# Performance work log

Hardware: AMD Instinct MI355X
Metric: run time of the kernel (lower is better)

Reference implementation:

```python
import jax, jax.numpy as jnp
import numpy as np

NUM_JOINTS = 75
COORDS = 3
HIDDEN = 256
MID = HIDDEN // 2
LN_EPS = 1e-5


def build_adjacency_matrix(num_joints=NUM_JOINTS):
    edges = []
    hand_bones = [(0, 1), (1, 2), (2, 3), (3, 4), (0, 5), (5, 6), (6, 7), (7, 8), (0, 9), (9, 10), (10, 11), (11, 12), (0, 13), (13, 14), (14, 15), (15, 16), (0, 17), (17, 18), (18, 19), (19, 20), (5, 9), (9, 13), (13, 17)]
    for i, j in hand_bones:
        edges.extend([(i, j), (j, i)])
    for i, j in hand_bones:
        edges.extend([(i + 21, j + 21), (j + 21, i + 21)])
    pose_bones = [(0, 1), (1, 2), (2, 3), (3, 7), (0, 4), (4, 5), (5, 6), (6, 8), (9, 10), (11, 12), (11, 13), (13, 15), (12, 14), (14, 16), (11, 23), (12, 24), (23, 24), (23, 25), (25, 27), (27, 29), (29, 31), (24, 26), (26, 28), (28, 30), (30, 32), (15, 17), (15, 19), (15, 21), (16, 18), (16, 20), (16, 22)]
    off = 42
    for i, j in pose_bones:
        if i < 33 and j < 33:
            edges.extend([(i + off, j + off), (j + off, i + off)])
    edges.extend([(57, 0), (0, 57), (58, 21), (21, 58)])
    A = np.zeros((num_joints, num_joints), dtype=np.float32)
    np.fill_diagonal(A, 1.0)
    for i, j in edges:
        if i < num_joints and j < num_joints:
            A[i, j] = 1.0
    deg = A.sum(axis=1)
    d = np.where(deg > 0, deg ** -0.5, 0.0).astype(np.float32)
    return (d[:, None] * A) * d[None, :]


def setup_inputs() -> dict:
    key = jax.random.key(0)
    ks = jax.random.split(key, 8)
    B = 16384
    x = jax.random.normal(ks[0], (B, NUM_JOINTS, COORDS), dtype=jnp.float32)
    A = jnp.asarray(build_adjacency_matrix())
    # Kaiming-uniform style init scales (values only need to be plausible)
    W1 = jax.random.normal(ks[1], (MID, COORDS), dtype=jnp.float32) * (1.0 / np.sqrt(COORDS))
    g1 = jnp.ones((MID,), jnp.float32)
    b1 = jnp.zeros((MID,), jnp.float32)
    W2 = jax.random.normal(ks[2], (HIDDEN, MID), dtype=jnp.float32) * (1.0 / np.sqrt(MID))
    g2 = jnp.ones((HIDDEN,), jnp.float32)
    b2 = jnp.zeros((HIDDEN,), jnp.float32)
    Wp = jax.random.normal(ks[3], (HIDDEN, COORDS), dtype=jnp.float32) * (1.0 / np.sqrt(COORDS))
    bp = jnp.zeros((HIDDEN,), jnp.float32)
    return {"x": x, "A": A, "W1": W1, "g1": g1, "b1": b1, "W2": W2, "g2": g2, "b2": b2, "Wp": Wp, "bp": bp}


def _layer_norm(h, gamma, beta):
    mu = h.mean(axis=-1, keepdims=True)
    var = ((h - mu) ** 2).mean(axis=-1, keepdims=True)
    return (h - mu) * jax.lax.rsqrt(var + LN_EPS) * gamma + beta


def _gcn(x, A, W, gamma, beta):
    # Z = A @ X @ W^T, then LayerNorm, then ReLU
    h = jnp.einsum('ij,bjc->bic', A, x)
    h = jnp.einsum('bic,oc->bio', h, W)
    return jax.nn.relu(_layer_norm(h, gamma, beta))


def reference(x, A, W1, g1, b1, W2, g2, b2, Wp, bp):
    # skip: per-frame mean of a linear projection of raw coords
    skip = (jnp.einsum('bjc,oc->bjo', x, Wp) + bp).mean(axis=1)  # (B, H)
    h = _gcn(x, A, W1, g1, b1)    # (B, 75, 128)
    h = _gcn(h, A, W2, g2, b2)    # (B, 75, 256)
    return h.mean(axis=1) + skip  # (B, 256)
```

## Files before the change

### kernel.cpp

```cpp
#include <hip/hip_runtime.h>

typedef __bf16 bf16;
typedef __bf16 bf16x4 __attribute__((ext_vector_type(4)));
typedef __bf16 bf16x8 __attribute__((ext_vector_type(8)));
typedef float  f32x2  __attribute__((ext_vector_type(2)));
typedef float  f32x4  __attribute__((ext_vector_type(4)));
typedef unsigned int u32;
typedef u32 u32x2 __attribute__((ext_vector_type(2)));
typedef u32 u32x4 __attribute__((ext_vector_type(4)));
typedef unsigned short u16;

#define NJ 75
#define SA 104
#define SH 104
#define SG 136
#define SX 104
#define SR 88
#define LN_EPS 1e-5f
#define MFMA16(a,b,c) __builtin_amdgcn_mfma_f32_16x16x32_bf16((a),(b),(c),0,0,0)

static __device__ __forceinline__ f32x4 f4z(){ f32x4 v={0.f,0.f,0.f,0.f}; return v; }
static __device__ __forceinline__ u32 pk2(float a, float b){
  u32 ua = (u32)__builtin_bit_cast(u16,(bf16)a);
  u32 ub = (u32)__builtin_bit_cast(u16,(bf16)b);
  return ua | (ub<<16);
}
static __device__ __forceinline__ float lo16f(u32 u){ return __uint_as_float(u<<16); }
static __device__ __forceinline__ float hi16f(u32 u){ return __uint_as_float(u & 0xffff0000u); }

template<int C>
static __device__ __forceinline__ float dppterm(float v){
  return __int_as_float(__builtin_amdgcn_update_dpp(0, __float_as_int(v), C, 0xF, 0xF, true));
}
static __device__ __forceinline__ float red16(float v){
  v += dppterm<0xB1>(v);
  v += dppterm<0x4E>(v);
  v += dppterm<0x141>(v);
  v += dppterm<0x140>(v);
  return v;
}

__global__ __launch_bounds__(512, 4)
void ke7(const float* __restrict__ gx,  const float* __restrict__ gA,
         const float* __restrict__ gW1, const float* __restrict__ gg1, const float* __restrict__ gb1,
         const float* __restrict__ gW2, const float* __restrict__ gg2, const float* __restrict__ gb2,
         const float* __restrict__ gWp, const float* __restrict__ gbp,
         float* __restrict__ gout, int B)
{
  __shared__ __align__(16) bf16 A_lds[80*SA];
  __shared__ __align__(16) bf16 h1[128*SH];
  __shared__ __align__(16) bf16 gss[80*SG];
  __shared__ __align__(16) bf16 xT[4*SX];
  __shared__ __align__(16) float reds[8*SR*2];
  __shared__ __align__(16) float fin[80*2];
  __shared__ __align__(16) float skl[4][256];
  __shared__ __align__(16) float b1l[128];
  __shared__ __align__(16) u32  g2b2[256];
  __shared__ __align__(16) bf16 W1l8[128*8];
  __shared__ __align__(16) u32x2 wpl[256];
  __shared__ __align__(16) float Msh[12];
  __shared__ float xbars[4];

  const int tid = threadIdx.x;
  const int w   = tid >> 6;
  const int l   = tid & 63;
  const int l16 = l & 15;
  const int lg  = l >> 4;

  for (int i = tid; i < 80*SA; i += 512) {
    const int r = i / SA, c = i - r*SA;
    A_lds[i] = (bf16)((r < NJ && c < NJ) ? gA[r*NJ + c] : 0.f);
  }
  for (int i = tid; i < 128*SH; i += 512) h1[i] = (bf16)0.f;
  for (int i = tid; i < 4*SX; i += 512) xT[i] = (bf16)0.f;
  if (tid < 128) {
    reds[tid*3+0] = gW1[tid*3+0];
    reds[tid*3+1] = gW1[tid*3+1];
    reds[tid*3+2] = gW1[tid*3+2];
    b1l[tid] = gb1[tid];
    fin[tid] = gg1[tid];
  }
  if (tid < 256) {
    g2b2[tid] = pk2(gg2[tid], gb2[tid]);
    u32x2 wv = { pk2(gWp[tid*3+0], gWp[tid*3+1]), pk2(gWp[tid*3+2], gbp[tid]) };
    wpl[tid] = wv;
  }
  __syncthreads();
  if (tid < 3) {
    float s = 0.f;
    for (int c = 0; c < 128; ++c) s += reds[c*3 + tid];
    Msh[6 + tid] = s * (1.f/128.f);
  }
  __syncthreads();
  if (tid < 128) {
    float wt0 = reds[tid*3+0] - Msh[6];
    float wt1 = reds[tid*3+1] - Msh[7];
    float wt2 = reds[tid*3+2] - Msh[8];
    const float g1v = fin[tid];
    W1l8[tid*8+0] = (bf16)(g1v*wt0);
    W1l8[tid*8+1] = (bf16)(g1v*wt1);
    W1l8[tid*8+2] = (bf16)(g1v*wt2);
    #pragma unroll
    for (int e = 3; e < 8; ++e) W1l8[tid*8+e] = (bf16)0.f;
    reds[tid*3+0] = wt0; reds[tid*3+1] = wt1; reds[tid*3+2] = wt2;
  }
  __syncthreads();
  if (tid < 6) {
    const int pa[6] = {0,1,2,0,0,1};
    const int pb[6] = {0,1,2,1,2,2};
    float s = 0.f;
    for (int c = 0; c < 128; ++c) s += reds[c*3 + pa[tid]] * reds[c*3 + pb[tid]];
    Msh[tid] = s * (1.f/128.f);
  }

  bf16x8 W2fr[2][4];
  #pragma unroll
  for (int ot = 0; ot < 2; ++ot) {
    const int o = 16*(2*w + ot) + l16;
    #pragma unroll
    for (int ks = 0; ks < 4; ++ks) {
      bf16x8 v;
      #pragma unroll
      for (int e = 0; e < 8; ++e) v[e] = (bf16)gW2[o*128 + 32*ks + 8*lg + e];
      W2fr[ot][ks] = v;
    }
  }
  __syncthreads();
  const float M00 = Msh[0], M11 = Msh[1], M22 = Msh[2];
  const float M01 = Msh[3], M02 = Msh[4], M12 = Msh[5];

  const int  fpb  = (B + 511) >> 9;
  const long base = (long)blockIdx.x * fpb;

  float xv[4] = {0.f, 0.f, 0.f, 0.f};
  if (w == 5) {
    long fg = base; if (fg >= B) fg = B - 1;
    #pragma unroll
    for (int k = 0; k < 4; ++k) { const int t = l + 64*k; if (t < 225) xv[k] = gx[fg*225 + t]; }
  }
  __syncthreads();

  f32x4 zacc[5][2];
  #pragma unroll
  for (int jt = 0; jt < 5; ++jt) { zacc[jt][0] = f4z(); zacc[jt][1] = f4z(); }

  const int nint = fpb + 2;
  for (int i = 0; i < nint; ++i) {
    if (i >= 1 && i <= fpb) {
      const bf16* hb = &h1[(16*w + l16)*SH];
      bf16x8 hf0 = *(const bf16x8*)&hb[ 0 + 8*lg];
      bf16x8 hf1 = *(const bf16x8*)&hb[32 + 8*lg];
      bf16x8 hf2 = *(const bf16x8*)&hb[64 + 8*lg];
      #pragma unroll
      for (int jt = 0; jt < 5; ++jt) {
        const bf16* ab = &A_lds[(16*jt + l16)*SA + 8*lg];
        f32x4 ag = f4z();
        ag = MFMA16(hf0, *(const bf16x8*)&ab[ 0], ag);
        ag = MFMA16(hf1, *(const bf16x8*)&ab[32], ag);
        ag = MFMA16(hf2, *(const bf16x8*)&ab[64], ag);
        bf16x4 p;
        #pragma unroll
        for (int r = 0; r < 4; ++r) p[r] = (bf16)ag[r];
        *(bf16x4*)&gss[(16*jt + l16)*SG + 16*w + 4*lg] = p;
      }
    }
    if (w == 5 && i < fpb) {
      float s0 = 0.f, s1 = 0.f, s2 = 0.f;
      #pragma unroll
      for (int k = 0; k < 4; ++k) {
        const int t = l + 64*k;
        if (t < 225) {
          const int j = (t*21846) >> 16;
          const int co = t - 3*j;
          xT[co*SX + j] = (bf16)xv[k];
          if (co == 0) s0 += xv[k]; else if (co == 1) s1 += xv[k]; else s2 += xv[k];
        }
      }
      s0 = red16(s0); s0 += __shfl_xor(s0, 16); s0 += __shfl_xor(s0, 32);
      s1 = red16(s1); s1 += __shfl_xor(s1, 16); s1 += __shfl_xor(s1, 32);
      s2 = red16(s2); s2 += __shfl_xor(s2, 16); s2 += __shfl_xor(s2, 32);
      if (l == 0) { xbars[0] = s0*(1.f/NJ); xbars[1] = s1*(1.f/NJ); xbars[2] = s2*(1.f/NJ); }
    }
    if (w == 6 && i >= 2) {
      float S = 0.f, Q = 0.f;
      #pragma unroll
      for (int ww = 0; ww < 8; ++ww) {
        const f32x2 a = *(const f32x2*)&reds[(ww*SR + l)*2];
        S += a[0]; Q += a[1];
      }
      const float mu = S * (1.f/256.f);
      const float rs = rsqrtf(Q * (1.f/256.f) - mu*mu + LN_EPS);
      f32x2 nr = { -mu*rs, rs };
      *(f32x2*)&fin[l*2] = nr;
    }
    if (w == 7 && i >= 2 && l < 16) {
      const int j2 = 64 + l;
      float S = 0.f, Q = 0.f;
      #pragma unroll
      for (int ww = 0; ww < 8; ++ww) {
        const f32x2 a = *(const f32x2*)&reds[(ww*SR + j2)*2];
        S += a[0]; Q += a[1];
      }
      const float mu = S * (1.f/256.f);
      const float rs = rsqrtf(Q * (1.f/256.f) - mu*mu + LN_EPS);
      f32x2 nr = { -mu*rs, rs };
      *(f32x2*)&fin[j2*2] = nr;
    }
    __syncthreads();

    if (i >= 2) {
      float nmv[5], rsv[5];
      #pragma unroll
      for (int jt = 0; jt < 5; ++jt) {
        const f32x2 nr = *(const f32x2*)&fin[(16*jt + l16)*2];
        nmv[jt] = nr[0]; rsv[jt] = nr[1];
      }
      float os[2][4];
      #pragma unroll
      for (int ot = 0; ot < 2; ++ot) {
        const u32x4 gb = *(const u32x4*)&g2b2[16*(2*w + ot) + 4*lg];
        #pragma unroll
        for (int r = 0; r < 4; ++r) os[ot][r] = 0.f;
        #pragma unroll
        for (int jt = 0; jt < 5; ++jt) {
          #pragma unroll
          for (int r = 0; r < 4; ++r) {
            float v = fmaf(fmaf(zacc[jt][ot][r], rsv[jt], nmv[jt]), lo16f(gb[r]), hi16f(gb[r]));
            v = fmaxf(v, 0.f);
            if (jt == 4) v = (l16 < 11) ? v : 0.f;
            os[ot][r] += v;
          }
        }
        #pragma unroll
        for (int r = 0; r < 4; ++r) os[ot][r] = red16(os[ot][r]);
      }
      const long f = base + (i - 2);
      if (l16 == 0 && f < B) {
        #pragma unroll
        for (int ot = 0; ot < 2; ++ot) {
          const int o0 = 16*(2*w + ot) + 4*lg;
          const f32x4 sk = *(const f32x4*)&skl[(i-2)&3][o0];
          f32x4 res;
          #pragma unroll
          for (int r = 0; r < 4; ++r) res[r] = os[ot][r]*(1.f/NJ) + sk[r];
          *(f32x4*)&gout[f*256 + o0] = res;
        }
      }
    }
    if (i >= 1 && i <= fpb) {
      #pragma unroll
      for (int jt = 0; jt < 5; ++jt) {
        const bf16* gr = &gss[(16*jt + l16)*SG + 8*lg];
        f32x4 z0 = f4z(), z1 = f4z();
        #pragma unroll
        for (int ks = 0; ks < 4; ++ks) {
          const bf16x8 gf = *(const bf16x8*)&gr[32*ks];
          z0 = MFMA16(W2fr[0][ks], gf, z0);
          z1 = MFMA16(W2fr[1][ks], gf, z1);
        }
        float s = 0.f, q = 0.f;
        #pragma unroll
        for (int r = 0; r < 4; ++r) {
          s += z0[r] + z1[r];
          q = fmaf(z0[r], z0[r], q); q = fmaf(z1[r], z1[r], q);
        }
        s += __shfl_xor(s, 16); q += __shfl_xor(q, 16);
        s += __shfl_xor(s, 32); q += __shfl_xor(q, 32);
        if (lg == 0) { f32x2 sq = {s, q}; *(f32x2*)&reds[(w*SR + 16*jt + l16)*2] = sq; }
        zacc[jt][0] = z0; zacc[jt][1] = z1;
      }
    }
    if (i < fpb && w < 5) {
      const int xrow = (l16 < 3) ? l16 : 3;
      const bf16* xb = &xT[xrow*SX + 8*lg];
      const bf16* ab = &A_lds[(16*w + l16)*SA + 8*lg];
      f32x4 at = f4z();
      at = MFMA16(*(const bf16x8*)&xb[ 0], *(const bf16x8*)&ab[ 0], at);
      at = MFMA16(*(const bf16x8*)&xb[32], *(const bf16x8*)&ab[32], at);
      at = MFMA16(*(const bf16x8*)&xb[64], *(const bf16x8*)&ab[64], at);
      const float a0 = at[0], a1 = at[1], a2 = at[2];
      float qd = fmaf(M00*a0, a0, fmaf(M11*a1, a1, fmaf(M22*a2, a2, LN_EPS)));
      qd = fmaf(2.f*M01*a0, a1, fmaf(2.f*M02*a0, a2, fmaf(2.f*M12*a1, a2, qd)));
      const float rs = rsqrtf(qd);
      bf16x8 hA;
      #pragma unroll
      for (int e = 0; e < 8; ++e) hA[e] = (bf16)0.f;
      hA[0] = (bf16)((lg == 0) ? a0*rs : 0.f);
      hA[1] = (bf16)((lg == 0) ? a1*rs : 0.f);
      hA[2] = (bf16)((lg == 0) ? a2*rs : 0.f);
      #pragma unroll
      for (int nt = 0; nt < 8; ++nt) {
        const bf16x8 wb = *(const bf16x8*)&W1l8[(16*nt + l16)*8];
        const f32x4 hp = MFMA16(hA, wb, f4z());
        const float b1v = b1l[16*nt + l16];
        bf16x4 pkk;
        #pragma unroll
        for (int r = 0; r < 4; ++r) pkk[r] = (bf16)fmaxf(hp[r] + b1v, 0.f);
        *(bf16x4*)&h1[(16*nt + l16)*SH + 16*w + 4*lg] = pkk;
      }
    }
    if (w == 5 && i + 1 < fpb) {
      long fg = base + i + 1; if (fg >= B) fg = B - 1;
      #pragma unroll
      for (int k = 0; k < 4; ++k) { const int t = l + 64*k; if (t < 225) xv[k] = gx[fg*225 + t]; }
    }
    if (w == 6 && i < fpb) {
      const float xb0 = xbars[0], xb1 = xbars[1], xb2 = xbars[2];
      #pragma unroll
      for (int k = 0; k < 4; ++k) {
        const int o = l + 64*k;
        const u32x2 wv = wpl[o];
        skl[i&3][o] = fmaf(lo16f(wv[0]), xb0, fmaf(hi16f(wv[0]), xb1, fmaf(lo16f(wv[1]), xb2, hi16f(wv[1]))));
      }
    }
    __syncthreads();
  }
}

extern "C" void kernel_launch(void* const* d_in, const int* in_sizes, int n_in,
                              void* d_out, int out_size, void* d_ws, size_t ws_size,
                              hipStream_t stream) {
  const float* x  = (const float*)d_in[0];
  const float* A  = (const float*)d_in[1];
  const float* W1 = (const float*)d_in[2];
  const float* g1 = (const float*)d_in[3];
  const float* b1 = (const float*)d_in[4];
  const float* W2 = (const float*)d_in[5];
  const float* g2 = (const float*)d_in[6];
  const float* b2 = (const float*)d_in[7];
  const float* Wp = (const float*)d_in[8];
  const float* bp = (const float*)d_in[9];
  float* out = (float*)d_out;
  const int B = in_sizes[0] / 225;
  ke7<<<dim3(512), dim3(512), 0, stream>>>(x, A, W1, g1, b1, W2, g2, b2, Wp, bp, out, B);
}
```

Baseline: 259.4 us.

## Interleave layer-2 epilogue with next frame's W2 MFMAs in steady state

In the steady-state iterations, the LayerNorm/ReLU/mean epilogue of the previous frame is fused into the same per-row-tile loop as the W2 MFMAs for the current frame. The aim is to let VALU epilogue work overlap with matrix-core work and to load the gss fragments early. Edge iterations keep the old separate paths. Launch bounds drop from 4 to 2 waves per SIMD, which gives the compiler more registers for the interleaved live state but may lower occupancy.

```diff
diff --git a/kernel.cpp b/kernel.cpp
--- a/kernel.cpp
+++ b/kernel.cpp
@@ -40,8 +40,8 @@
   return v;
 }
 
-__global__ __launch_bounds__(512, 4)
-void ke7(const float* __restrict__ gx,  const float* __restrict__ gA,
+__global__ __launch_bounds__(512, 2)
+void ke9(const float* __restrict__ gx,  const float* __restrict__ gA,
          const float* __restrict__ gW1, const float* __restrict__ gg1, const float* __restrict__ gb1,
          const float* __restrict__ gW2, const float* __restrict__ gg2, const float* __restrict__ gb2,
          const float* __restrict__ gWp, const float* __restrict__ gbp,
@@ -208,32 +208,50 @@
     }
     __syncthreads();
 
-    if (i >= 2) {
-      float nmv[5], rsv[5];
+    if (i >= 2 && i <= fpb) {
+      float os[2][4];
+      #pragma unroll
+      for (int ot = 0; ot < 2; ++ot)
+        #pragma unroll
+        for (int r = 0; r < 4; ++r) os[ot][r] = 0.f;
+      const u32x4 gb0 = *(const u32x4*)&g2b2[16*(2*w + 0) + 4*lg];
+      const u32x4 gb1 = *(const u32x4*)&g2b2[16*(2*w + 1) + 4*lg];
       #pragma unroll
       for (int jt = 0; jt < 5; ++jt) {
+        const bf16* gr = &gss[(16*jt + l16)*SG + 8*lg];
+        const bf16x8 gf0 = *(const bf16x8*)&gr[ 0];
+        const bf16x8 gf1 = *(const bf16x8*)&gr[32];
+        const bf16x8 gf2 = *(const bf16x8*)&gr[64];
+        const bf16x8 gf3 = *(const bf16x8*)&gr[96];
         const f32x2 nr = *(const f32x2*)&fin[(16*jt + l16)*2];
-        nmv[jt] = nr[0]; rsv[jt] = nr[1];
-      }
-      float os[2][4];
-      #pragma unroll
-      for (int ot = 0; ot < 2; ++ot) {
-        const u32x4 gb = *(const u32x4*)&g2b2[16*(2*w + ot) + 4*lg];
-        #pragma unroll
-        for (int r = 0; r < 4; ++r) os[ot][r] = 0.f;
-        #pragma unroll
-        for (int jt = 0; jt < 5; ++jt) {
-          #pragma unroll
-          for (int r = 0; r < 4; ++r) {
-            float v = fmaf(fmaf(zacc[jt][ot][r], rsv[jt], nmv[jt]), lo16f(gb[r]), hi16f(gb[r]));
-            v = fmaxf(v, 0.f);
-            if (jt == 4) v = (l16 < 11) ? v : 0.f;
-            os[ot][r] += v;
-          }
-        }
+        #pragma unroll
+        for (int r = 0; r < 4; ++r) {
+          float v0 = fmaf(fmaf(zacc[jt][0][r], nr[1], nr[0]), lo16f(gb0[r]), hi16f(gb0[r]));
+          float v1 = fmaf(fmaf(zacc[jt][1][r], nr[1], nr[0]), lo16f(gb1[r]), hi16f(gb1[r]));
+          v0 = fmaxf(v0, 0.f); v1 = fmaxf(v1, 0.f);
+          if (jt == 4) { v0 = (l16 < 11) ? v0 : 0.f; v1 = (l16 < 11) ? v1 : 0.f; }
+          os[0][r] += v0; os[1][r] += v1;
+        }
+        f32x4 z0 = f4z(), z1 = f4z();
+        z0 = MFMA16(W2fr[0][0], gf0, z0); z1 = MFMA16(W2fr[1][0], gf0, z1);
+        z0 = MFMA16(W2fr[0][1], gf1, z0); z1 = MFMA16(W2fr[1][1], gf1, z1);
+        z0 = MFMA16(W2fr[0][2], gf2, z0); z1 = MFMA16(W2fr[1][2], gf2, z1);
+        z0 = MFMA16(W2fr[0][3], gf3, z0); z1 = MFMA16(W2fr[1][3], gf3, z1);
+        float s = 0.f, q = 0.f;
+        #pragma unroll
+        for (int r = 0; r < 4; ++r) {
+          s += z0[r] + z1[r];
+          q = fmaf(z0[r], z0[r], q); q = fmaf(z1[r], z1[r], q);
+        }
+        s += __shfl_xor(s, 16); q += __shfl_xor(q, 16);
+        s += __shfl_xor(s, 32); q += __shfl_xor(q, 32);
+        if (lg == 0) { f32x2 sq = {s, q}; *(f32x2*)&reds[(w*SR + 16*jt + l16)*2] = sq; }
+        zacc[jt][0] = z0; zacc[jt][1] = z1;
+      }
+      #pragma unroll
+      for (int ot = 0; ot < 2; ++ot)
         #pragma unroll
         for (int r = 0; r < 4; ++r) os[ot][r] = red16(os[ot][r]);
-      }
       const long f = base + (i - 2);
       if (l16 == 0 && f < B) {
         #pragma unroll
@@ -246,28 +264,68 @@
           *(f32x4*)&gout[f*256 + o0] = res;
         }
       }
-    }
-    if (i >= 1 && i <= fpb) {
-      #pragma unroll
-      for (int jt = 0; jt < 5; ++jt) {
-        const bf16* gr = &gss[(16*jt + l16)*SG + 8*lg];
-        f32x4 z0 = f4z(), z1 = f4z();
-        #pragma unroll
-        for (int ks = 0; ks < 4; ++ks) {
-          const bf16x8 gf = *(const bf16x8*)&gr[32*ks];
-          z0 = MFMA16(W2fr[0][ks], gf, z0);
-          z1 = MFMA16(W2fr[1][ks], gf, z1);
-        }
-        float s = 0.f, q = 0.f;
-        #pragma unroll
-        for (int r = 0; r < 4; ++r) {
-          s += z0[r] + z1[r];
-          q = fmaf(z0[r], z0[r], q); q = fmaf(z1[r], z1[r], q);
-        }
-        s += __shfl_xor(s, 16); q += __shfl_xor(q, 16);
-        s += __shfl_xor(s, 32); q += __shfl_xor(q, 32);
-        if (lg == 0) { f32x2 sq = {s, q}; *(f32x2*)&reds[(w*SR + 16*jt + l16)*2] = sq; }
-        zacc[jt][0] = z0; zacc[jt][1] = z1;
+    } else {
+      if (i >= 2) {
+        float nmv[5], rsv[5];
+        #pragma unroll
+        for (int jt = 0; jt < 5; ++jt) {
+          const f32x2 nr = *(const f32x2*)&fin[(16*jt + l16)*2];
+          nmv[jt] = nr[0]; rsv[jt] = nr[1];
+        }
+        float os[2][4];
+        #pragma unroll
+        for (int ot = 0; ot < 2; ++ot) {
+          const u32x4 gb = *(const u32x4*)&g2b2[16*(2*w + ot) + 4*lg];
+          #pragma unroll
+          for (int r = 0; r < 4; ++r) os[ot][r] = 0.f;
+          #pragma unroll
+          for (int jt = 0; jt < 5; ++jt) {
+            #pragma unroll
+            for (int r = 0; r < 4; ++r) {
+              float v = fmaf(fmaf(zacc[jt][ot][r], rsv[jt], nmv[jt]), lo16f(gb[r]), hi16f(gb[r]));
+              v = fmaxf(v, 0.f);
+              if (jt == 4) v = (l16 < 11) ? v : 0.f;
+              os[ot][r] += v;
+            }
+          }
+          #pragma unroll
+          for (int r = 0; r < 4; ++r) os[ot][r] = red16(os[ot][r]);
+        }
+        const long f = base + (i - 2);
+        if (l16 == 0 && f < B) {
+          #pragma unroll
+          for (int ot = 0; ot < 2; ++ot) {
+            const int o0 = 16*(2*w + ot) + 4*lg;
+            const f32x4 sk = *(const f32x4*)&skl[(i-2)&3][o0];
+            f32x4 res;
+            #pragma unroll
+            for (int r = 0; r < 4; ++r) res[r] = os[ot][r]*(1.f/NJ) + sk[r];
+            *(f32x4*)&gout[f*256 + o0] = res;
+          }
+        }
+      }
+      if (i >= 1 && i <= fpb) {
+        #pragma unroll
+        for (int jt = 0; jt < 5; ++jt) {
+          const bf16* gr = &gss[(16*jt + l16)*SG + 8*lg];
+          f32x4 z0 = f4z(), z1 = f4z();
+          #pragma unroll
+          for (int ks = 0; ks < 4; ++ks) {
+            const bf16x8 gf = *(const bf16x8*)&gr[32*ks];
+            z0 = MFMA16(W2fr[0][ks], gf, z0);
+            z1 = MFMA16(W2fr[1][ks], gf, z1);
+          }
+          float s = 0.f, q = 0.f;
+          #pragma unroll
+          for (int r = 0; r < 4; ++r) {
+            s += z0[r] + z1[r];
+            q = fmaf(z0[r], z0[r], q); q = fmaf(z1[r], z1[r], q);
+          }
+          s += __shfl_xor(s, 16); q += __shfl_xor(q, 16);
+          s += __shfl_xor(s, 32); q += __shfl_xor(q, 32);
+          if (lg == 0) { f32x2 sq = {s, q}; *(f32x2*)&reds[(w*SR + 16*jt + l16)*2] = sq; }
+          zacc[jt][0] = z0; zacc[jt][1] = z1;
+        }
       }
     }
     if (i < fpb && w < 5) {
@@ -332,5 +390,5 @@
   const float* bp = (const float*)d_in[9];
   float* out = (float*)d_out;
   const int B = in_sizes[0] / 225;
-  ke7<<<dim3(512), dim3(512), 0, stream>>>(x, A, W1, g1, b1, W2, g2, b2, Wp, bp, out, B);
-}
+  ke9<<<dim3(512), dim3(512), 0, stream>>>(x, A, W1, g1, b1, W2, g2, b2, Wp, bp, out, B);
+}
```

Measured after the change: 297.8 us. 14.8% more time.
